# Kernel tuning notes

Measured on AMD Instinct MI355X. Metric: run time of the kernel, lower is better.

## Reference

```python
import jax, jax.numpy as jnp
import numpy as np

NEG_SLOPE = 0.2  # GATConv default negative_slope

N_NODES = 50000
N_EDGES = 1250000
D_IN = 64
D_OUT = 64


def setup_inputs() -> dict:
    key = jax.random.key(0)
    ks = jax.random.split(key, 5)
    x = jax.random.normal(ks[0], (N_NODES, D_IN), dtype=jnp.float32)
    edge_index = jax.random.randint(ks[1], (2, N_EDGES), 0, N_NODES, dtype=jnp.int64)
    W = jax.random.normal(ks[2], (D_IN, D_OUT), dtype=jnp.float32) / np.sqrt(D_IN)
    att_src = jax.random.normal(ks[3], (D_OUT,), dtype=jnp.float32) / np.sqrt(D_OUT)
    att_dst = jax.random.normal(ks[4], (D_OUT,), dtype=jnp.float32) / np.sqrt(D_OUT)
    bias = jnp.zeros((D_OUT,), dtype=jnp.float32)
    return {"x": x, "edge_index": edge_index, "W": W,
            "att_src": att_src, "att_dst": att_dst, "bias": bias}


def reference(x, edge_index, W, att_src, att_dst, bias):
    n = x.shape[0]
    # add self loops (GATConv default add_self_loops=True)
    loop = jnp.arange(n, dtype=edge_index.dtype)
    src = jnp.concatenate([edge_index[0], loop])
    dst = jnp.concatenate([edge_index[1], loop])

    h = x @ W                                   # [N, D_OUT]
    a_src = h @ att_src                         # [N]
    a_dst = h @ att_dst                         # [N]

    e = a_src[src] + a_dst[dst]                 # [E+N]
    e = jnp.where(e >= 0, e, NEG_SLOPE * e)     # leaky relu

    # softmax over incoming edges of each destination node
    e_max = jax.ops.segment_max(e, dst, num_segments=n)
    ex = jnp.exp(e - e_max[dst])
    denom = jax.ops.segment_sum(ex, dst, num_segments=n)
    alpha = ex / denom[dst]                     # [E+N]

    # scatter-aggregate messages
    out = jax.ops.segment_sum(alpha[:, None] * h[src], dst, num_segments=n)
    return out + bias
```

## Files before the change

### kernel.cpp

```cpp
#include <hip/hip_runtime.h>

#define N_NODES 50000
#define N_EDGES 1250000
#define D 64
#define NEG_SLOPE 0.2f
#define N_TOT (N_EDGES + N_NODES)

__global__ void k_detect(const unsigned int* ei_raw, int* flag) {
    if (threadIdx.x == 0 && blockIdx.x == 0) {
        int is64 = 1;
        for (int i = 1; i < 128; i += 2)
            if (ei_raw[i] != 0u) { is64 = 0; break; }
        *flag = is64;
    }
}

__device__ __forceinline__ int get_idx(const void* ei, long long pos, int is64) {
    if (is64) return (int)((const long long*)ei)[pos];
    return ((const int*)ei)[pos];
}

__global__ void k_init(float* __restrict__ out, float* __restrict__ denom,
                       const float* __restrict__ bias) {
    int t = blockIdx.x * blockDim.x + threadIdx.x;
    if (t < N_NODES * D) {
        out[t] = bias[t & (D - 1)];
        if (t < N_NODES) denom[t] = 0.f;
    }
}

__global__ __launch_bounds__(256) void k_gemm(
        const float* __restrict__ x, const float* __restrict__ W,
        const float* __restrict__ att_src, const float* __restrict__ att_dst,
        float* __restrict__ h, float* __restrict__ a_src, float* __restrict__ a_dst) {
    __shared__ float Ws[D * D];
    __shared__ float xs[4][D];
    const int tid  = threadIdx.x;
    const int lane = tid & 63;
    const int wave = tid >> 6;

    for (int i = tid; i < D * D; i += 256) Ws[i] = W[i];
    const float as = att_src[lane];
    const float ad = att_dst[lane];
    __syncthreads();

    const int ngroups = (N_NODES + 3) / 4;
    for (int g = blockIdx.x; g < ngroups; g += gridDim.x) {
        const int row = g * 4 + wave;
        __syncthreads();
        if (row < N_NODES) xs[wave][lane] = x[(long long)row * D + lane];
        __syncthreads();
        if (row < N_NODES) {
            float acc = 0.f;
#pragma unroll
            for (int k = 0; k < D; ++k)
                acc += xs[wave][k] * Ws[k * D + lane];
            h[(long long)row * D + lane] = acc;
            float vs = acc * as, vd = acc * ad;
#pragma unroll
            for (int off = 32; off > 0; off >>= 1) {
                vs += __shfl_down(vs, off);
                vd += __shfl_down(vd, off);
            }
            if (lane == 0) { a_src[row] = vs; a_dst[row] = vd; }
        }
    }
}

__global__ void k_edge1(const void* __restrict__ ei, const int* __restrict__ flag,
                        const float* __restrict__ a_src, const float* __restrict__ a_dst,
                        float* __restrict__ ex, float* __restrict__ denom) {
    const long long e = (long long)blockIdx.x * blockDim.x + threadIdx.x;
    if (e >= N_TOT) return;
    const int is64 = *flag;
    int s, d;
    if (e < N_EDGES) {
        s = get_idx(ei, e, is64);
        d = get_idx(ei, (long long)N_EDGES + e, is64);
    } else {
        s = d = (int)(e - N_EDGES);
    }
    float v = a_src[s] + a_dst[d];
    v = (v >= 0.f) ? v : NEG_SLOPE * v;
    const float xv = expf(v);
    ex[e] = xv;
    atomicAdd(&denom[d], xv);
}

__global__ void k_edge2(const void* __restrict__ ei, const int* __restrict__ flag,
                        const float* __restrict__ ex, const float* __restrict__ denom,
                        const float* __restrict__ h, float* __restrict__ out) {
    const long long gid = (long long)blockIdx.x * blockDim.x + threadIdx.x;
    const long long e = gid >> 6;
    const int lane = threadIdx.x & 63;
    if (e >= N_TOT) return;
    const int is64 = *flag;
    int s, d;
    if (e < N_EDGES) {
        s = get_idx(ei, e, is64);
        d = get_idx(ei, (long long)N_EDGES + e, is64);
    } else {
        s = d = (int)(e - N_EDGES);
    }
    const float alpha = ex[e] / denom[d];
    const float hv = h[(long long)s * D + lane];
    atomicAdd(&out[(long long)d * D + lane], alpha * hv);
}

extern "C" void kernel_launch(void* const* d_in, const int* in_sizes, int n_in,
                              void* d_out, int out_size, void* d_ws, size_t ws_size,
                              hipStream_t stream) {
    const float* x       = (const float*)d_in[0];
    const void*  ei      = d_in[1];
    const float* W       = (const float*)d_in[2];
    const float* att_src = (const float*)d_in[3];
    const float* att_dst = (const float*)d_in[4];
    const float* bias    = (const float*)d_in[5];
    float* out = (float*)d_out;

    char* ws = (char*)d_ws;
    int*   flag  = (int*)ws;
    float* h     = (float*)(ws + 64);
    float* a_src = h + (size_t)N_NODES * D;
    float* a_dst = a_src + N_NODES;
    float* denom = a_dst + N_NODES;
    float* ex    = denom + N_NODES;

    k_detect<<<1, 1, 0, stream>>>((const unsigned int*)ei, flag);
    k_init<<<(N_NODES * D + 255) / 256, 256, 0, stream>>>(out, denom, bias);
    k_gemm<<<1024, 256, 0, stream>>>(x, W, att_src, att_dst, h, a_src, a_dst);
    k_edge1<<<(N_TOT + 255) / 256, 256, 0, stream>>>(ei, flag, a_src, a_dst, ex, denom);
    const long long e2_threads = (long long)N_TOT * 64;
    k_edge2<<<(unsigned int)((e2_threads + 255) / 256), 256, 0, stream>>>(
        ei, flag, ex, denom, h, out);
}
```

Before: 433.2 us.

## Build CSR by destination and aggregate per node without float atomics

Replaces the per-edge atomic scatter of 64-wide messages with a CSR build: a histogram of destinations, a single-block prefix scan, and a scatter of source ids and exp scores into destination-sorted slots. One wavefront per node then sums the softmax denominator and accumulates weighted source rows in registers, writing each output row once with the bias. This removes about 84M float atomics to the output. It adds three extra passes over the edges, a serial one-block scan, and a nondeterministic edge order within each node. As in the previous version, no max is subtracted before exp.

```diff
diff --git a/kernel.cpp b/kernel.cpp
--- a/kernel.cpp
+++ b/kernel.cpp
@@ -20,13 +20,9 @@
     return ((const int*)ei)[pos];
 }
 
-__global__ void k_init(float* __restrict__ out, float* __restrict__ denom,
-                       const float* __restrict__ bias) {
+__global__ void k_zero(int* __restrict__ count) {
     int t = blockIdx.x * blockDim.x + threadIdx.x;
-    if (t < N_NODES * D) {
-        out[t] = bias[t & (D - 1)];
-        if (t < N_NODES) denom[t] = 0.f;
-    }
+    if (t < N_NODES) count[t] = 0;
 }
 
 __global__ __launch_bounds__(256) void k_gemm(
@@ -67,9 +63,52 @@
     }
 }
 
-__global__ void k_edge1(const void* __restrict__ ei, const int* __restrict__ flag,
-                        const float* __restrict__ a_src, const float* __restrict__ a_dst,
-                        float* __restrict__ ex, float* __restrict__ denom) {
+__global__ void k_hist(const void* __restrict__ ei, const int* __restrict__ flag,
+                       int* __restrict__ count) {
+    const long long e = (long long)blockIdx.x * blockDim.x + threadIdx.x;
+    if (e >= N_TOT) return;
+    const int is64 = *flag;
+    const int d = (e < N_EDGES) ? get_idx(ei, (long long)N_EDGES + e, is64)
+                                : (int)(e - N_EDGES);
+    atomicAdd(&count[d], 1);
+}
+
+__global__ __launch_bounds__(1024) void k_scan(const int* __restrict__ count,
+                                               int* __restrict__ rowptr,
+                                               int* __restrict__ cursor) {
+    __shared__ int part[1024];
+    const int t = threadIdx.x;
+    const int CHUNK = (N_NODES + 1023) / 1024;
+    const int base = t * CHUNK;
+    int sum = 0;
+    for (int i = 0; i < CHUNK; ++i) {
+        const int idx = base + i;
+        if (idx < N_NODES) sum += count[idx];
+    }
+    part[t] = sum;
+    __syncthreads();
+    for (int off = 1; off < 1024; off <<= 1) {
+        int v = (t >= off) ? part[t - off] : 0;
+        __syncthreads();
+        part[t] += v;
+        __syncthreads();
+    }
+    int run = (t == 0) ? 0 : part[t - 1];
+    for (int i = 0; i < CHUNK; ++i) {
+        const int idx = base + i;
+        if (idx < N_NODES) {
+            rowptr[idx] = run;
+            cursor[idx] = run;
+            run += count[idx];
+        }
+    }
+    if (t == 1023) rowptr[N_NODES] = part[1023];
+}
+
+__global__ void k_scatter(const void* __restrict__ ei, const int* __restrict__ flag,
+                          const float* __restrict__ a_src, const float* __restrict__ a_dst,
+                          int* __restrict__ cursor,
+                          int* __restrict__ srcs, float* __restrict__ vals) {
     const long long e = (long long)blockIdx.x * blockDim.x + threadIdx.x;
     if (e >= N_TOT) return;
     const int is64 = *flag;
@@ -82,29 +121,42 @@
     }
     float v = a_src[s] + a_dst[d];
     v = (v >= 0.f) ? v : NEG_SLOPE * v;
-    const float xv = expf(v);
-    ex[e] = xv;
-    atomicAdd(&denom[d], xv);
+    const int pos = atomicAdd(&cursor[d], 1);
+    srcs[pos] = s;
+    vals[pos] = expf(v);
 }
 
-__global__ void k_edge2(const void* __restrict__ ei, const int* __restrict__ flag,
-                        const float* __restrict__ ex, const float* __restrict__ denom,
-                        const float* __restrict__ h, float* __restrict__ out) {
-    const long long gid = (long long)blockIdx.x * blockDim.x + threadIdx.x;
-    const long long e = gid >> 6;
+__global__ __launch_bounds__(256) void k_agg(
+        const int* __restrict__ rowptr, const int* __restrict__ srcs,
+        const float* __restrict__ vals, const float* __restrict__ h,
+        const float* __restrict__ bias, float* __restrict__ out) {
+    const int node = (int)((blockIdx.x * (long long)blockDim.x + threadIdx.x) >> 6);
     const int lane = threadIdx.x & 63;
-    if (e >= N_TOT) return;
-    const int is64 = *flag;
-    int s, d;
-    if (e < N_EDGES) {
-        s = get_idx(ei, e, is64);
-        d = get_idx(ei, (long long)N_EDGES + e, is64);
-    } else {
-        s = d = (int)(e - N_EDGES);
+    if (node >= N_NODES) return;
+    const int beg = rowptr[node];
+    const int end = rowptr[node + 1];
+
+    float part = 0.f;
+    for (int i = beg + lane; i < end; i += 64) part += vals[i];
+#pragma unroll
+    for (int off = 32; off > 0; off >>= 1) part += __shfl_xor(part, off);
+    const float inv = 1.f / part;
+
+    float acc = 0.f;
+    int i = beg;
+    for (; i + 4 <= end; i += 4) {
+        const int s0 = srcs[i], s1 = srcs[i + 1], s2 = srcs[i + 2], s3 = srcs[i + 3];
+        const float a0 = vals[i] * inv, a1 = vals[i + 1] * inv,
+                    a2 = vals[i + 2] * inv, a3 = vals[i + 3] * inv;
+        acc += a0 * h[(long long)s0 * D + lane];
+        acc += a1 * h[(long long)s1 * D + lane];
+        acc += a2 * h[(long long)s2 * D + lane];
+        acc += a3 * h[(long long)s3 * D + lane];
     }
-    const float alpha = ex[e] / denom[d];
-    const float hv = h[(long long)s * D + lane];
-    atomicAdd(&out[(long long)d * D + lane], alpha * hv);
+    for (; i < end; ++i)
+        acc += (vals[i] * inv) * h[(long long)srcs[i] * D + lane];
+
+    out[(long long)node * D + lane] = acc + bias[lane];
 }
 
 extern "C" void kernel_launch(void* const* d_in, const int* in_sizes, int n_in,
@@ -119,18 +171,23 @@
     float* out = (float*)d_out;
 
     char* ws = (char*)d_ws;
-    int*   flag  = (int*)ws;
-    float* h     = (float*)(ws + 64);
-    float* a_src = h + (size_t)N_NODES * D;
-    float* a_dst = a_src + N_NODES;
-    float* denom = a_dst + N_NODES;
-    float* ex    = denom + N_NODES;
+    int*   flag   = (int*)ws;
+    float* h      = (float*)(ws + 64);
+    float* a_src  = h + (size_t)N_NODES * D;
+    float* a_dst  = a_src + N_NODES;
+    int*   count  = (int*)(a_dst + N_NODES);
+    int*   rowptr = count + N_NODES;
+    int*   cursor = rowptr + N_NODES + 1;
+    int*   srcs   = cursor + N_NODES;
+    float* vals   = (float*)(srcs + N_TOT);
 
     k_detect<<<1, 1, 0, stream>>>((const unsigned int*)ei, flag);
-    k_init<<<(N_NODES * D + 255) / 256, 256, 0, stream>>>(out, denom, bias);
+    k_zero<<<(N_NODES + 255) / 256, 256, 0, stream>>>(count);
     k_gemm<<<1024, 256, 0, stream>>>(x, W, att_src, att_dst, h, a_src, a_dst);
-    k_edge1<<<(N_TOT + 255) / 256, 256, 0, stream>>>(ei, flag, a_src, a_dst, ex, denom);
-    const long long e2_threads = (long long)N_TOT * 64;
-    k_edge2<<<(unsigned int)((e2_threads + 255) / 256), 256, 0, stream>>>(
-        ei, flag, ex, denom, h, out);
+    k_hist<<<(N_TOT + 255) / 256, 256, 0, stream>>>(ei, flag, count);
+    k_scan<<<1, 1024, 0, stream>>>(count, rowptr, cursor);
+    k_scatter<<<(N_TOT + 255) / 256, 256, 0, stream>>>(ei, flag, a_src, a_dst,
+                                                       cursor, srcs, vals);
+    k_agg<<<(int)(((long long)N_NODES * 64 + 255) / 256), 256, 0, stream>>>(
+        rowptr, srcs, vals, h, bias, out);
 }
```

Result: faster. 359.9 us (-16.9%).
